# Performance work log

Hardware: AMD Instinct MI355X
Metric: run time of the kernel (lower is better)

The kernel has to match this reference:

```python
import jax, jax.numpy as jnp
import numpy as np

NUM_NODES = 100000
NUM_EDGES = 640000
IN_DIM = 128
OUT_DIM = 128
NUM_REL = 16


def setup_inputs() -> dict:
    key = jax.random.key(0)
    k1, k2, k3, k4, k5 = jax.random.split(key, 5)
    x = jax.random.normal(k1, (NUM_NODES, IN_DIM), dtype=jnp.float32)
    edge_index = jax.random.randint(k2, (2, NUM_EDGES), 0, NUM_NODES, dtype=jnp.int64)
    edge_types = jax.random.randint(k3, (NUM_EDGES,), 0, NUM_REL, dtype=jnp.int64)
    # xavier-uniform-ish params
    rw_bound = float(np.sqrt(6.0 / (IN_DIM * OUT_DIM + NUM_REL)))
    relation_weights = jax.random.uniform(k4, (NUM_REL, IN_DIM, OUT_DIM), dtype=jnp.float32, minval=-rw_bound, maxval=rw_bound)
    sw_bound = float(np.sqrt(6.0 / (IN_DIM + OUT_DIM)))
    self_weight = jax.random.uniform(k5, (IN_DIM, OUT_DIM), dtype=jnp.float32, minval=-sw_bound, maxval=sw_bound)
    bias = jnp.zeros((OUT_DIM,), dtype=jnp.float32)
    return {
        'x': x,
        'edge_index': edge_index,
        'edge_types': edge_types,
        'relation_weights': relation_weights,
        'self_weight': self_weight,
        'bias': bias,
    }


def reference(x, edge_index, edge_types, relation_weights, self_weight, bias):
    num_nodes = x.shape[0]
    # self loop transform: (N, out)
    self_msg = x @ self_weight
    # transform all nodes by every relation weight once: (R, N, out)
    transformed = jnp.einsum('ni,rio->rno', x, relation_weights)
    src = edge_index[0]
    dst = edge_index[1]
    # per-edge message: pick (relation, source) transformed feature -> (E, out)
    msgs = transformed[edge_types, src]
    # scatter-add into destination nodes
    neighbor_msg = jax.ops.segment_sum(msgs, dst, num_segments=num_nodes)
    # dropout=0.0 (eval) -> identity
    return jax.nn.relu(self_msg + neighbor_msg + bias)
```

## Files before the change

### kernel.cpp

```cpp
#include <hip/hip_runtime.h>

#define N_NODES 100000
#define N_EDGES 640000
#define IN_DIM  128
#define OUT_DIM 128
#define N_REL   16
#define EPB     64
#define MEPB    128
#define SELF_PAD 100096
#define MAX_SLOTS (SELF_PAD + N_EDGES + 2048)
#define SENT    (N_EDGES + N_NODES)
#define MSG_ROWS (N_EDGES + N_NODES + 128)
#define NB_SCAN ((N_NODES + 255) / 256)
#define CVT_XB  (N_NODES * IN_DIM / 4 / 256)
#define CVT_WB  (17 * 16384 / 256)
#define HIST_B  ((N_EDGES + 255) / 256)
#define SELF_B  (SELF_PAD / 256)

typedef unsigned short u16;
typedef unsigned int   u32;
typedef __attribute__((ext_vector_type(8))) short bf16x8;
typedef __attribute__((ext_vector_type(4))) float f32x4;

__device__ inline u16 f2bf(float f) {
    u32 u = __builtin_bit_cast(u32, f);
    return (u16)((u + 0x7fffu + ((u >> 16) & 1u)) >> 16);
}
__device__ inline float bf2f(u16 s) {
    u32 u = ((u32)s) << 16;
    return __builtin_bit_cast(float, u);
}

__global__ __launch_bounds__(256) void k_pre(const float* __restrict__ x,
                                             const float* __restrict__ rw,
                                             const float* __restrict__ sw,
                                             const int* __restrict__ etype,
                                             const int* __restrict__ dst,
                                             u16* __restrict__ xb,
                                             u16* __restrict__ wt,
                                             int* __restrict__ counts_rel,
                                             int* __restrict__ dst_count,
                                             int* __restrict__ sorted) {
    int b = blockIdx.x, t = threadIdx.x;
    if (b < CVT_XB) {
        int i = b * 256 + t;
        float4 v = ((const float4*)x)[i];
        ushort4 p; p.x = f2bf(v.x); p.y = f2bf(v.y); p.z = f2bf(v.z); p.w = f2bf(v.w);
        ((ushort4*)xb)[i] = p;
    } else if (b < CVT_XB + CVT_WB) {
        int i = (b - CVT_XB) * 256 + t;
        int r = i >> 14, rem = i & 16383;
        int k = rem >> 7, np = rem & 127;
        float v = (r < 16) ? rw[i] : sw[rem];
        int c = np >> 4, nn = np & 15, kk = k >> 5, q = (k >> 3) & 3, j = k & 7;
        wt[(size_t)r * 16384 + (c * 4 + kk) * 512 + (q * 16 + nn) * 8 + j] = f2bf(v);
    } else if (b < CVT_XB + CVT_WB + HIST_B) {
        __shared__ int bins[N_REL];
        if (t < N_REL) bins[t] = 0;
        __syncthreads();
        int e = (b - CVT_XB - CVT_WB) * 256 + t;
        if (e < N_EDGES) {
            atomicAdd(&bins[etype[e]], 1);
            atomicAdd(&dst_count[dst[e]], 1);
        }
        __syncthreads();
        if (t < N_REL && bins[t]) atomicAdd(&counts_rel[t], bins[t]);
    } else {
        int i = (b - CVT_XB - CVT_WB - HIST_B) * 256 + t;
        sorted[i] = (i < N_NODES) ? (N_EDGES + i) : SENT;
    }
}

__global__ __launch_bounds__(256) void k_scan1(const int* __restrict__ dst_count,
                                               int* __restrict__ row_ptr,
                                               int* __restrict__ part) {
    __shared__ int buf[2][256];
    int t = threadIdx.x;
    int i = blockIdx.x * 256 + t;
    int v = (i < N_NODES) ? (dst_count[i] + 1) : 0;
    buf[0][t] = v;
    __syncthreads();
    int cur = 0;
    #pragma unroll
    for (int off = 1; off < 256; off <<= 1) {
        int nxt = cur ^ 1;
        int s = buf[cur][t];
        if (t >= off) s += buf[cur][t - off];
        buf[nxt][t] = s;
        __syncthreads();
        cur = nxt;
    }
    int inc = buf[cur][t];
    if (i < N_NODES) row_ptr[i] = inc - v;
    if (t == 255) part[blockIdx.x] = inc;
}

__global__ __launch_bounds__(512) void k_mid2(int* __restrict__ part,
                                              const int* __restrict__ counts,
                                              int* __restrict__ cursor,
                                              int* __restrict__ seg,
                                              int* __restrict__ sorted) {
    int t = threadIdx.x;
    if (blockIdx.x == 0) {
        __shared__ int buf[2][512];
        int v = (t < NB_SCAN) ? part[t] : 0;
        buf[0][t] = v;
        __syncthreads();
        int cur = 0;
        #pragma unroll
        for (int off = 1; off < 512; off <<= 1) {
            int nxt = cur ^ 1;
            int s = buf[cur][t];
            if (t >= off) s += buf[cur][t - off];
            buf[nxt][t] = s;
            __syncthreads();
            cur = nxt;
        }
        int inc = buf[cur][t];
        if (t < NB_SCAN) part[t] = inc - v;
    } else {
        __shared__ int s_seg[N_REL + 1];
        if (t == 0) {
            int s = SELF_PAD;
            for (int r = 0; r < N_REL; ++r) {
                cursor[r] = s; seg[r] = s; s_seg[r] = s;
                s += (counts[r] + 127) & ~127;
            }
            seg[N_REL] = s; s_seg[N_REL] = s;
        }
        __syncthreads();
        for (int r = 0; r < N_REL; ++r) {
            int b = s_seg[r] + counts[r], e2 = s_seg[r + 1];
            if (b + t < e2) sorted[b + t] = SENT;
        }
        for (int i = s_seg[N_REL] + t; i < MAX_SLOTS; i += 512)
            sorted[i] = SENT;
    }
}

__global__ __launch_bounds__(256) void k_scan3(int* __restrict__ row_ptr,
                                               const int* __restrict__ part,
                                               int* __restrict__ cursor_dst) {
    int t = threadIdx.x;
    int i = blockIdx.x * 256 + t;
    if (i < N_NODES) {
        int r = row_ptr[i] + part[blockIdx.x];
        row_ptr[i] = r;
        cursor_dst[i] = r + 1;
    }
    if (i == 0) row_ptr[N_NODES] = N_EDGES + N_NODES;
}

__global__ __launch_bounds__(256) void k_scatter_rel(const int* __restrict__ etype,
                                                     int* __restrict__ cursor,
                                                     int* __restrict__ sorted) {
    __shared__ int bins[N_REL];
    __shared__ int base[N_REL];
    int t = threadIdx.x;
    if (t < N_REL) bins[t] = 0;
    __syncthreads();
    int e = blockIdx.x * 256 + t;
    int rel = 0;
    bool valid = (e < N_EDGES);
    if (valid) { rel = etype[e]; atomicAdd(&bins[rel], 1); }
    __syncthreads();
    if (t < N_REL) {
        base[t] = bins[t] ? atomicAdd(&cursor[t], bins[t]) : 0;
        bins[t] = 0;
    }
    __syncthreads();
    if (valid) {
        int p = atomicAdd(&bins[rel], 1);
        sorted[base[rel] + p] = e;
    }
}

__global__ __launch_bounds__(256, 4) void k_msg_mfma(const u16* __restrict__ xb,
                                                     const u16* __restrict__ wt,
                                                     const int* __restrict__ src,
                                                     const int* __restrict__ etype,
                                                     const int* __restrict__ dst,
                                                     const int* __restrict__ sorted,
                                                     const int* __restrict__ row_ptr,
                                                     int* __restrict__ cursor_dst,
                                                     u16* __restrict__ msgs) {
    __shared__ u16 s_w[128 * 128];
    __shared__ int s_src[MEPB], s_pos[MEPB];
    int t = threadIdx.x;
    int e0 = blockIdx.x * MEPB;

    int ee0 = sorted[e0];
    int relb = (ee0 < N_EDGES) ? etype[ee0] : N_REL;
    const uint4* wsrc = (const uint4*)(wt + (size_t)relb * 16384);
    for (int i = t; i < 2048; i += 256)
        *(uint4*)&s_w[i * 8] = wsrc[i];
    if (t < MEPB) {
        int eid = sorted[e0 + t];
        int sv, pv;
        if (eid < N_EDGES) {
            sv = src[eid];
            pv = atomicAdd(&cursor_dst[dst[eid]], 1);
        } else if (eid < SENT) {
            sv = eid - N_EDGES;
            pv = row_ptr[sv];
        } else {
            sv = 0;
            pv = SENT + ((e0 + t) & 127);
        }
        s_src[t] = sv; s_pos[t] = pv;
    }
    __syncthreads();

    int wv = t >> 6, lane = t & 63;
    int n = lane & 15, q = lane >> 4;
    int eb = wv * 32;

    bf16x8 bx[2][4];
    int p[2];
    #pragma unroll
    for (int g = 0; g < 2; ++g) {
        int en = eb + g * 16 + n;
        const u16* xrow = xb + (size_t)s_src[en] * 128 + q * 8;
        p[g] = s_pos[en];
        #pragma unroll
        for (int kk = 0; kk < 4; ++kk)
            bx[g][kk] = *(const bf16x8*)(xrow + kk * 32);
    }

    uint4 uv[2][4];
    #pragma unroll
    for (int c = 0; c < 8; ++c) {
        bf16x8 aw[4];
        #pragma unroll
        for (int kk = 0; kk < 4; ++kk)
            aw[kk] = *(const bf16x8*)&s_w[(c * 4 + kk) * 512 + lane * 8];
        #pragma unroll
        for (int g = 0; g < 2; ++g) {
            f32x4 acc = {0.f, 0.f, 0.f, 0.f};
            #pragma unroll
            for (int kk = 0; kk < 4; ++kk)
                acc = __builtin_amdgcn_mfma_f32_16x16x32_bf16(aw[kk], bx[g][kk], acc, 0, 0, 0);
            u32 lo = (u32)f2bf(acc[0]) | ((u32)f2bf(acc[1]) << 16);
            u32 hi = (u32)f2bf(acc[2]) | ((u32)f2bf(acc[3]) << 16);
            if ((c & 1) == 0) { uv[g][c >> 1].x = lo; uv[g][c >> 1].y = hi; }
            else              { uv[g][c >> 1].z = lo; uv[g][c >> 1].w = hi; }
        }
    }
    #pragma unroll
    for (int g = 0; g < 2; ++g) {
        u32* mrow = (u32*)(msgs + (size_t)p[g] * 128 + q * 32);
        #pragma unroll
        for (int j = 0; j < 4; ++j)
            *(uint4*)(mrow + j * 4) = uv[g][j];
    }
}

__global__ __launch_bounds__(256) void k_gather(const int* __restrict__ row_ptr,
                                                const u16* __restrict__ msgs,
                                                const float* __restrict__ bias,
                                                float* __restrict__ out) {
    int wid  = (blockIdx.x * 256 + threadIdx.x) >> 6;
    int lane = threadIdx.x & 63;
    if (wid >= N_NODES) return;
    int r0 = row_ptr[wid], r1 = row_ptr[wid + 1];
    int h = lane & 15, quarter = lane >> 4;
    const uint4* m = (const uint4*)msgs;
    float s[8] = {0.f,0.f,0.f,0.f,0.f,0.f,0.f,0.f};
    for (int i = r0 + quarter; i < r1; i += 4) {
        uint4 v = m[(size_t)i * 16 + h];
        s[0] += bf2f((u16)(v.x & 0xffffu)); s[1] += bf2f((u16)(v.x >> 16));
        s[2] += bf2f((u16)(v.y & 0xffffu)); s[3] += bf2f((u16)(v.y >> 16));
        s[4] += bf2f((u16)(v.z & 0xffffu)); s[5] += bf2f((u16)(v.z >> 16));
        s[6] += bf2f((u16)(v.w & 0xffffu)); s[7] += bf2f((u16)(v.w >> 16));
    }
    #pragma unroll
    for (int j = 0; j < 8; ++j) {
        s[j] += __shfl_xor(s[j], 16);
        s[j] += __shfl_xor(s[j], 32);
    }
    if (quarter == 0) {
        int c0 = (2 * h) & 7, c1 = (2 * h + 1) & 7, qq = h >> 2;
        float4 b0 = *(const float4*)&bias[c0 * 16 + qq * 4];
        float4 b1 = *(const float4*)&bias[c1 * 16 + qq * 4];
        float* ob = out + (size_t)wid * 128;
        float4 v0, v1;
        v0.x = fmaxf(s[0] + b0.x, 0.f); v0.y = fmaxf(s[1] + b0.y, 0.f);
        v0.z = fmaxf(s[2] + b0.z, 0.f); v0.w = fmaxf(s[3] + b0.w, 0.f);
        v1.x = fmaxf(s[4] + b1.x, 0.f); v1.y = fmaxf(s[5] + b1.y, 0.f);
        v1.z = fmaxf(s[6] + b1.z, 0.f); v1.w = fmaxf(s[7] + b1.w, 0.f);
        *(float4*)(ob + c0 * 16 + qq * 4) = v0;
        *(float4*)(ob + c1 * 16 + qq * 4) = v1;
    }
}

__global__ __launch_bounds__(128) void k_self_old(const float* __restrict__ x,
                                                  const float* __restrict__ sw,
                                                  const float* __restrict__ bias,
                                                  float* __restrict__ out) {
    __shared__ float s_x[8][IN_DIM];
    int t = threadIdx.x;
    int n0 = blockIdx.x * 8;
    for (int i = t; i < 8 * IN_DIM; i += 128) {
        int r = i >> 7, j = i & 127;
        s_x[r][j] = x[(size_t)(n0 + r) * IN_DIM + j];
    }
    __syncthreads();
    float acc[8] = {0.f,0.f,0.f,0.f,0.f,0.f,0.f,0.f};
    for (int k = 0; k < IN_DIM; ++k) {
        float w = sw[k * OUT_DIM + t];
        #pragma unroll
        for (int i = 0; i < 8; ++i) acc[i] += s_x[i][k] * w;
    }
    float b = bias[t];
    #pragma unroll
    for (int i = 0; i < 8; ++i)
        out[(size_t)(n0 + i) * OUT_DIM + t] = acc[i] + b;
}

__global__ __launch_bounds__(256) void k_hist_rel(const int* __restrict__ etype,
                                                  int* __restrict__ counts_rel) {
    __shared__ int bins[N_REL];
    int t = threadIdx.x;
    if (t < N_REL) bins[t] = 0;
    __syncthreads();
    int e = blockIdx.x * 256 + t;
    if (e < N_EDGES) atomicAdd(&bins[etype[e]], 1);
    __syncthreads();
    if (t < N_REL && bins[t]) atomicAdd(&counts_rel[t], bins[t]);
}

__global__ void k_scan_rel(const int* __restrict__ counts, int* __restrict__ cursor) {
    if (threadIdx.x == 0) {
        int s = 0;
        for (int r = 0; r < N_REL; ++r) { cursor[r] = s; s += counts[r]; }
    }
}

__global__ __launch_bounds__(256) void k_edge_atomic(const float* __restrict__ x,
                                              const float* __restrict__ rw,
                                              const int* __restrict__ src,
                                              const int* __restrict__ dst,
                                              const int* __restrict__ etype,
                                              const int* __restrict__ sorted,
                                              float* __restrict__ out) {
    __shared__ int s_src[EPB], s_dst[EPB], s_rel[EPB];
    __shared__ float s_x[EPB][IN_DIM];
    int t = threadIdx.x;
    int e0 = blockIdx.x * EPB;
    if (t < EPB) {
        int eid = sorted[e0 + t];
        s_src[t] = src[eid]; s_dst[t] = dst[eid]; s_rel[t] = etype[eid];
    }
    __syncthreads();
    for (int i = t; i < EPB * IN_DIM; i += 256) {
        int e = i >> 7, j = i & 127;
        s_x[e][j] = x[(size_t)s_src[e] * IN_DIM + j];
    }
    int rel0 = s_rel[0];
    bool uni = true;
    for (int i = 1; i < EPB; ++i) uni &= (s_rel[i] == rel0);
    __syncthreads();
    int cg = t & 31, eg = t >> 5;
    for (int i = 0; i < 8; ++i) {
        int e = eg * 8 + i;
        int rel = uni ? rel0 : s_rel[e];
        const float4* Wr = (const float4*)(rw + (size_t)rel * IN_DIM * OUT_DIM);
        float a0=0.f, a1=0.f, a2=0.f, a3=0.f;
        for (int k = 0; k < 128; ++k) {
            float4 w = Wr[k * 32 + cg];
            float xv = s_x[e][k];
            a0 += xv * w.x; a1 += xv * w.y; a2 += xv * w.z; a3 += xv * w.w;
        }
        float* o = out + (size_t)s_dst[e] * OUT_DIM + cg * 4;
        atomicAdd(o + 0, a0); atomicAdd(o + 1, a1);
        atomicAdd(o + 2, a2); atomicAdd(o + 3, a3);
    }
}

__global__ void k_relu(float* __restrict__ out) {
    int i = blockIdx.x * blockDim.x + threadIdx.x;
    float4* o4 = (float4*)out;
    const int n4 = N_NODES * OUT_DIM / 4;
    if (i < n4) {
        float4 v = o4[i];
        v.x = fmaxf(v.x, 0.f); v.y = fmaxf(v.y, 0.f);
        v.z = fmaxf(v.z, 0.f); v.w = fmaxf(v.w, 0.f);
        o4[i] = v;
    }
}

extern "C" void kernel_launch(void* const* d_in, const int* in_sizes, int n_in,
                              void* d_out, int out_size, void* d_ws, size_t ws_size,
                              hipStream_t stream) {
    const float* x     = (const float*)d_in[0];
    const int*   eidx  = (const int*)d_in[1];
    const int*   etype = (const int*)d_in[2];
    const float* rw    = (const float*)d_in[3];
    const float* sw    = (const float*)d_in[4];
    const float* bias  = (const float*)d_in[5];
    float* out = (float*)d_out;
    const int* src = eidx;
    const int* dst = eidx + N_EDGES;

    int* counts_rel = (int*)d_ws;
    int* cursor_rel = counts_rel + 16;
    int* seg        = cursor_rel + 16;
    int* part       = seg + 32;
    int* dst_count  = part + 512;
    int* row_ptr    = dst_count + N_NODES;
    int* cursor_dst = row_ptr + N_NODES + 1;
    int* sorted     = cursor_dst + N_NODES;
    size_t off = (((char*)(sorted + MAX_SLOTS) - (char*)d_ws) + 255) & ~(size_t)255;
    u16* xb   = (u16*)((char*)d_ws + off);
    u16* wtb  = xb + (size_t)N_NODES * 128;
    u16* msgs = wtb + 17 * 16384;
    size_t need = (size_t)((char*)(msgs + (size_t)MSG_ROWS * 128) - (char*)d_ws);

    const int MB = MAX_SLOTS / MEPB;

    if (ws_size >= need) {
        hipMemsetAsync(d_ws, 0, (size_t)(576 + N_NODES) * sizeof(int), stream);
        k_pre<<<CVT_XB + CVT_WB + HIST_B + SELF_B, 256, 0, stream>>>(
            x, rw, sw, etype, dst, xb, wtb, counts_rel, dst_count, sorted);
        k_scan1<<<NB_SCAN, 256, 0, stream>>>(dst_count, row_ptr, part);
        k_mid2<<<2, 512, 0, stream>>>(part, counts_rel, cursor_rel, seg, sorted);
        k_scan3<<<NB_SCAN, 256, 0, stream>>>(row_ptr, part, cursor_dst);
        k_scatter_rel<<<HIST_B, 256, 0, stream>>>(etype, cursor_rel, sorted);

        k_msg_mfma<<<MB, 256, 0, stream>>>(xb, wtb, src, etype, dst, sorted,
                                           row_ptr, cursor_dst, msgs);
        k_gather<<<(N_NODES * 64 + 255) / 256, 256, 0, stream>>>(row_ptr, msgs, bias, out);
    } else {
        hipMemsetAsync(counts_rel, 0, 16 * sizeof(int), stream);
        k_hist_rel<<<HIST_B, 256, 0, stream>>>(etype, counts_rel);
        k_scan_rel<<<1, 64, 0, stream>>>(counts_rel, cursor_rel);
        k_scatter_rel<<<HIST_B, 256, 0, stream>>>(etype, cursor_rel, sorted);
        k_self_old<<<N_NODES / 8, 128, 0, stream>>>(x, sw, bias, out);
        k_edge_atomic<<<N_EDGES / EPB, 256, 0, stream>>>(x, rw, src, dst, etype, sorted, out);
        k_relu<<<(N_NODES * OUT_DIM / 4 + 255) / 256, 256, 0, stream>>>(out);
    }
}
```

Measured before the change: 327.4 us.

## Fuse scan3 with relation scatter, double message tile, unroll gather loop

Merges the row-pointer fixup and the relation-bucket scatter into one launch, which removes a kernel launch and the gap between the two. It doubles the edges per message block to 256 with 512 threads so each staged relation weight tile is reused over more edges, and widens segment padding to match. It also unrolls the gather loop by two to keep more loads in flight. Larger blocks raise register and LDS pressure and add padding waste at relation segment boundaries.

```diff
diff --git a/kernel.cpp b/kernel.cpp
--- a/kernel.cpp
+++ b/kernel.cpp
@@ -6,11 +6,11 @@
 #define OUT_DIM 128
 #define N_REL   16
 #define EPB     64
-#define MEPB    128
+#define MEPB    256
 #define SELF_PAD 100096
-#define MAX_SLOTS (SELF_PAD + N_EDGES + 2048)
+#define MAX_SLOTS (SELF_PAD + N_EDGES + 4096)
 #define SENT    (N_EDGES + N_NODES)
-#define MSG_ROWS (N_EDGES + N_NODES + 128)
+#define MSG_ROWS (N_EDGES + N_NODES + 256)
 #define NB_SCAN ((N_NODES + 255) / 256)
 #define CVT_XB  (N_NODES * IN_DIM / 4 / 256)
 #define CVT_WB  (17 * 16384 / 256)
@@ -124,7 +124,7 @@
             int s = SELF_PAD;
             for (int r = 0; r < N_REL; ++r) {
                 cursor[r] = s; seg[r] = s; s_seg[r] = s;
-                s += (counts[r] + 127) & ~127;
+                s += (counts[r] + 255) & ~255;
             }
             seg[N_REL] = s; s_seg[N_REL] = s;
         }
@@ -138,44 +138,44 @@
     }
 }
 
-__global__ __launch_bounds__(256) void k_scan3(int* __restrict__ row_ptr,
-                                               const int* __restrict__ part,
-                                               int* __restrict__ cursor_dst) {
-    int t = threadIdx.x;
-    int i = blockIdx.x * 256 + t;
-    if (i < N_NODES) {
-        int r = row_ptr[i] + part[blockIdx.x];
-        row_ptr[i] = r;
-        cursor_dst[i] = r + 1;
-    }
-    if (i == 0) row_ptr[N_NODES] = N_EDGES + N_NODES;
-}
-
-__global__ __launch_bounds__(256) void k_scatter_rel(const int* __restrict__ etype,
-                                                     int* __restrict__ cursor,
-                                                     int* __restrict__ sorted) {
-    __shared__ int bins[N_REL];
-    __shared__ int base[N_REL];
-    int t = threadIdx.x;
-    if (t < N_REL) bins[t] = 0;
-    __syncthreads();
-    int e = blockIdx.x * 256 + t;
-    int rel = 0;
-    bool valid = (e < N_EDGES);
-    if (valid) { rel = etype[e]; atomicAdd(&bins[rel], 1); }
-    __syncthreads();
-    if (t < N_REL) {
-        base[t] = bins[t] ? atomicAdd(&cursor[t], bins[t]) : 0;
-        bins[t] = 0;
-    }
-    __syncthreads();
-    if (valid) {
-        int p = atomicAdd(&bins[rel], 1);
-        sorted[base[rel] + p] = e;
-    }
-}
-
-__global__ __launch_bounds__(256, 4) void k_msg_mfma(const u16* __restrict__ xb,
+__global__ __launch_bounds__(256) void k_scan3_scatter(int* __restrict__ row_ptr,
+                                                       const int* __restrict__ part,
+                                                       int* __restrict__ cursor_dst,
+                                                       const int* __restrict__ etype,
+                                                       int* __restrict__ cursor_rel,
+                                                       int* __restrict__ sorted) {
+    int t = threadIdx.x;
+    if (blockIdx.x < NB_SCAN) {
+        int i = blockIdx.x * 256 + t;
+        if (i < N_NODES) {
+            int r = row_ptr[i] + part[blockIdx.x];
+            row_ptr[i] = r;
+            cursor_dst[i] = r + 1;
+        }
+        if (i == 0) row_ptr[N_NODES] = N_EDGES + N_NODES;
+    } else {
+        __shared__ int bins[N_REL];
+        __shared__ int base[N_REL];
+        if (t < N_REL) bins[t] = 0;
+        __syncthreads();
+        int e = (blockIdx.x - NB_SCAN) * 256 + t;
+        int rel = 0;
+        bool valid = (e < N_EDGES);
+        if (valid) { rel = etype[e]; atomicAdd(&bins[rel], 1); }
+        __syncthreads();
+        if (t < N_REL) {
+            base[t] = bins[t] ? atomicAdd(&cursor_rel[t], bins[t]) : 0;
+            bins[t] = 0;
+        }
+        __syncthreads();
+        if (valid) {
+            int p = atomicAdd(&bins[rel], 1);
+            sorted[base[rel] + p] = e;
+        }
+    }
+}
+
+__global__ __launch_bounds__(512, 4) void k_msg_mfma(const u16* __restrict__ xb,
                                                      const u16* __restrict__ wt,
                                                      const int* __restrict__ src,
                                                      const int* __restrict__ etype,
@@ -192,7 +192,7 @@
     int ee0 = sorted[e0];
     int relb = (ee0 < N_EDGES) ? etype[ee0] : N_REL;
     const uint4* wsrc = (const uint4*)(wt + (size_t)relb * 16384);
-    for (int i = t; i < 2048; i += 256)
+    for (int i = t; i < 2048; i += 512)
         *(uint4*)&s_w[i * 8] = wsrc[i];
     if (t < MEPB) {
         int eid = sorted[e0 + t];
@@ -205,7 +205,7 @@
             pv = row_ptr[sv];
         } else {
             sv = 0;
-            pv = SENT + ((e0 + t) & 127);
+            pv = SENT + ((e0 + t) & 255);
         }
         s_src[t] = sv; s_pos[t] = pv;
     }
@@ -266,7 +266,20 @@
     int h = lane & 15, quarter = lane >> 4;
     const uint4* m = (const uint4*)msgs;
     float s[8] = {0.f,0.f,0.f,0.f,0.f,0.f,0.f,0.f};
-    for (int i = r0 + quarter; i < r1; i += 4) {
+    int i = r0 + quarter;
+    for (; i + 4 < r1; i += 8) {
+        uint4 v = m[(size_t)i * 16 + h];
+        uint4 w = m[(size_t)(i + 4) * 16 + h];
+        s[0] += bf2f((u16)(v.x & 0xffffu)); s[1] += bf2f((u16)(v.x >> 16));
+        s[2] += bf2f((u16)(v.y & 0xffffu)); s[3] += bf2f((u16)(v.y >> 16));
+        s[4] += bf2f((u16)(v.z & 0xffffu)); s[5] += bf2f((u16)(v.z >> 16));
+        s[6] += bf2f((u16)(v.w & 0xffffu)); s[7] += bf2f((u16)(v.w >> 16));
+        s[0] += bf2f((u16)(w.x & 0xffffu)); s[1] += bf2f((u16)(w.x >> 16));
+        s[2] += bf2f((u16)(w.y & 0xffffu)); s[3] += bf2f((u16)(w.y >> 16));
+        s[4] += bf2f((u16)(w.z & 0xffffu)); s[5] += bf2f((u16)(w.z >> 16));
+        s[6] += bf2f((u16)(w.w & 0xffffu)); s[7] += bf2f((u16)(w.w >> 16));
+    }
+    if (i < r1) {
         uint4 v = m[(size_t)i * 16 + h];
         s[0] += bf2f((u16)(v.x & 0xffffu)); s[1] += bf2f((u16)(v.x >> 16));
         s[2] += bf2f((u16)(v.y & 0xffffu)); s[3] += bf2f((u16)(v.y >> 16));
@@ -333,6 +346,30 @@
     if (threadIdx.x == 0) {
         int s = 0;
         for (int r = 0; r < N_REL; ++r) { cursor[r] = s; s += counts[r]; }
+    }
+}
+
+__global__ __launch_bounds__(256) void k_scatter_rel(const int* __restrict__ etype,
+                                                     int* __restrict__ cursor,
+                                                     int* __restrict__ sorted) {
+    __shared__ int bins[N_REL];
+    __shared__ int base[N_REL];
+    int t = threadIdx.x;
+    if (t < N_REL) bins[t] = 0;
+    __syncthreads();
+    int e = blockIdx.x * 256 + t;
+    int rel = 0;
+    bool valid = (e < N_EDGES);
+    if (valid) { rel = etype[e]; atomicAdd(&bins[rel], 1); }
+    __syncthreads();
+    if (t < N_REL) {
+        base[t] = bins[t] ? atomicAdd(&cursor[t], bins[t]) : 0;
+        bins[t] = 0;
+    }
+    __syncthreads();
+    if (valid) {
+        int p = atomicAdd(&bins[rel], 1);
+        sorted[base[rel] + p] = e;
     }
 }
 
@@ -424,10 +461,10 @@
             x, rw, sw, etype, dst, xb, wtb, counts_rel, dst_count, sorted);
         k_scan1<<<NB_SCAN, 256, 0, stream>>>(dst_count, row_ptr, part);
         k_mid2<<<2, 512, 0, stream>>>(part, counts_rel, cursor_rel, seg, sorted);
-        k_scan3<<<NB_SCAN, 256, 0, stream>>>(row_ptr, part, cursor_dst);
-        k_scatter_rel<<<HIST_B, 256, 0, stream>>>(etype, cursor_rel, sorted);
-
-        k_msg_mfma<<<MB, 256, 0, stream>>>(xb, wtb, src, etype, dst, sorted,
+        k_scan3_scatter<<<NB_SCAN + HIST_B, 256, 0, stream>>>(
+            row_ptr, part, cursor_dst, etype, cursor_rel, sorted);
+
+        k_msg_mfma<<<MB, 512, 0, stream>>>(xb, wtb, src, etype, dst, sorted,
                                            row_ptr, cursor_dst, msgs);
         k_gather<<<(N_NODES * 64 + 255) / 256, 256, 0, stream>>>(row_ptr, msgs, bias, out);
     } else {
```

Result: slower. 334.7 us (+2.2%).
